# Optimization experiments

Measured on AMD Instinct MI355X. Metric: run time of the kernel, lower is better.

The kernel has to match this reference:

```python
import jax, jax.numpy as jnp
import numpy as np

VOCAB, EMB, HID, NTAG, T = 32000, 1024, 1024, 5, 4096
H2 = HID // 2
START, STOP = 3, 4
NEG = -10000.0


def setup_inputs() -> dict:
    key = jax.random.key(0)
    ks = jax.random.split(key, 14)
    sentence = jax.random.randint(ks[0], (T,), 0, VOCAB)
    emb = jax.random.normal(ks[1], (VOCAB, EMB), jnp.float32) * 0.02
    W_ih_f = jax.random.normal(ks[2], (4 * H2, EMB), jnp.float32) * 0.02
    W_hh_f = jax.random.normal(ks[3], (4 * H2, H2), jnp.float32) * 0.02
    b_f = jax.random.normal(ks[4], (4 * H2,), jnp.float32) * 0.02
    W_ih_b = jax.random.normal(ks[5], (4 * H2, EMB), jnp.float32) * 0.02
    W_hh_b = jax.random.normal(ks[6], (4 * H2, H2), jnp.float32) * 0.02
    b_b = jax.random.normal(ks[7], (4 * H2,), jnp.float32) * 0.02
    W_out = jax.random.normal(ks[8], (NTAG, HID), jnp.float32) * 0.02
    b_out = jax.random.normal(ks[9], (NTAG,), jnp.float32) * 0.02
    transitions = jax.random.normal(ks[10], (NTAG, NTAG), jnp.float32)
    transitions = transitions.at[START, :].set(NEG).at[:, STOP].set(NEG)
    h0 = jax.random.normal(ks[11], (2, 1, H2), jnp.float32)
    c0 = jax.random.normal(ks[12], (2, 1, H2), jnp.float32)
    return dict(sentence=sentence, emb=emb, W_ih_f=W_ih_f, W_hh_f=W_hh_f, b_f=b_f,
                W_ih_b=W_ih_b, W_hh_b=W_hh_b, b_b=b_b, W_out=W_out, b_out=b_out,
                transitions=transitions, h0=h0, c0=c0)


def _lstm_scan(x, h0, c0, W_ih, W_hh, b):
    # x: [T, EMB]; PyTorch gate order i, f, g, o
    def step(carry, xt):
        h, c = carry
        g = W_ih @ xt + W_hh @ h + b  # [4*H2]
        i, f, gg, o = jnp.split(g, 4)
        c2 = jax.nn.sigmoid(f) * c + jax.nn.sigmoid(i) * jnp.tanh(gg)
        h2 = jax.nn.sigmoid(o) * jnp.tanh(c2)
        return (h2, c2), h2
    _, hs = jax.lax.scan(step, (h0, c0), x)
    return hs  # [T, H2]


def _viterbi(feats, transitions):
    init = jnp.full((NTAG,), NEG, jnp.float32).at[START].set(0.0)

    def vstep(fv, feat):
        ntv = fv[None, :] + transitions          # [to, from]
        bptr = jnp.argmax(ntv, axis=1)
        return jnp.max(ntv, axis=1) + feat, bptr

    fv, bptrs = jax.lax.scan(vstep, init, feats)  # bptrs: [T, NTAG]
    terminal = fv + transitions[STOP]
    best_tag = jnp.argmax(terminal)
    score = terminal[best_tag]

    def back(tag, bp):
        prev = bp[tag]
        return prev, prev

    _, path_rev = jax.lax.scan(back, best_tag, bptrs[::-1])
    # path_rev[::-1] = [START, tag_1, ..., tag_{T-1}]; drop START, append best_tag
    path = jnp.concatenate([path_rev[::-1][1:], best_tag[None]])
    return score, path


def reference(sentence, emb, W_ih_f, W_hh_f, b_f, W_ih_b, W_hh_b, b_b,
              W_out, b_out, transitions, h0, c0):
    x = emb[sentence]  # [T, EMB]
    hf = _lstm_scan(x, h0[0, 0], c0[0, 0], W_ih_f, W_hh_f, b_f)
    hb = _lstm_scan(x[::-1], h0[1, 0], c0[1, 0], W_ih_b, W_hh_b, b_b)[::-1]
    lstm_out = jnp.concatenate([hf, hb], axis=-1)          # [T, HID]
    feats = lstm_out @ W_out.T + b_out                     # [T, NTAG]
    score, path = _viterbi(feats, transitions)
    return score, path
```

## Files before the change

### kernel.cpp

```cpp
#include <hip/hip_runtime.h>
#include <hip/hip_bf16.h>
#include <math.h>

#define TSEQ 4096
#define EMBD 1024
#define HH   512
#define NTAGS 5
#define NGATE 2048
#define NEGV (-10000.0f)
#define START_TAG 3
#define STOP_TAG 4
#define LSTM_WGS 64
#define PROJ_WGS 1024
#define VIT_BLOCK (LSTM_WGS + PROJ_WGS)

typedef unsigned long long u64;
typedef unsigned int u32;

__device__ __forceinline__ float sigm(float x){ return 1.0f/(1.0f+expf(-x)); }

__device__ __forceinline__ u64 pack_pair(float h, u32 tag){
  return ((u64)tag << 32) | (u64)__float_as_uint(h);
}
__device__ __forceinline__ float rdlane_f(float v, int l){
  return __uint_as_float((u32)__builtin_amdgcn_readlane(__float_as_uint(v), l));
}

__global__ void k_init(const float* __restrict__ h0, u64* __restrict__ hx2,
                       int* __restrict__ rdy){
  int tid = threadIdx.x;
  if (tid < 1024){
    int dir = tid >> 9, u = tid & 511;
    hx2[(dir*2 + 0)*HH + u] = pack_pair(h0[dir*HH + u], 0u);
    hx2[(dir*2 + 1)*HH + u] = pack_pair(0.f, 0xFFFFFFFFu);
  }
  if (tid < 96) rdy[tid] = 0;
}

__global__ __launch_bounds__(512, 2) void k_fused(
    const int* __restrict__ sent, const float* __restrict__ emb,
    const float* __restrict__ Wif, const float* __restrict__ bf,
    const float* __restrict__ Wib, const float* __restrict__ bb,
    const float* __restrict__ Whf, const float* __restrict__ Whb,
    const float* __restrict__ c0, const float* __restrict__ Wout,
    const float* __restrict__ bout, const float* __restrict__ trans,
    float* __restrict__ A, float* __restrict__ hseq, float* __restrict__ feats,
    int* __restrict__ bpw, float* __restrict__ out,
    u64* __restrict__ hx2, int* __restrict__ rdy){
  __shared__ __align__(16) char smem[17408];
  const int tid = threadIdx.x;

  if (blockIdx.x == VIT_BLOCK){
    if (tid >= 64) return;
    const int lane = tid;
    while (__hip_atomic_load(&rdy[66], __ATOMIC_ACQUIRE, __HIP_MEMORY_SCOPE_AGENT) < LSTM_WGS)
      __builtin_amdgcn_s_sleep(8);
    float*  sf  = (float*)smem;
    float4* sf4 = (float4*)smem;
    const float4* gf4 = (const float4*)feats;
    const int rr = (lane < 5) ? lane : 0;
    const float Tr0 = trans[rr*NTAGS+0], Tr1 = trans[rr*NTAGS+1],
                Tr2 = trans[rr*NTAGS+2], Tr3 = trans[rr*NTAGS+3],
                Tr4 = trans[rr*NTAGS+4];
    const float S0=trans[STOP_TAG*NTAGS+0], S1=trans[STOP_TAG*NTAGS+1],
                S2=trans[STOP_TAG*NTAGS+2], S3=trans[STOP_TAG*NTAGS+3],
                S4=trans[STOP_TAG*NTAGS+4];
    float fv0 = NEGV, fv1 = NEGV, fv2 = NEGV, fv3 = 0.f, fv4 = NEGV;

    for (int c = 0; c < TSEQ/512; c++){
      #pragma unroll
      for (int i = 0; i < 16; i++)
        sf4[i*64 + lane] = gf4[(size_t)c*1024 + i*64 + lane];
      asm volatile("s_waitcnt vmcnt(0) lgkmcnt(0)" ::: "memory");
      for (int tt = 0; tt < 512; tt++){
        const float featr = sf[tt*8 + rr];
        const float n0 = fv0 + Tr0, n1 = fv1 + Tr1, n2 = fv2 + Tr2,
                    n3 = fv3 + Tr3, n4 = fv4 + Tr4;
        const float m  = fmaxf(fmaxf(fmaxf(n0, n1), fmaxf(n2, n3)), n4);
        const int idx  = (n0 == m) ? 0 : ((n1 == m) ? 1 : ((n2 == m) ? 2 :
                         ((n3 == m) ? 3 : 4)));
        const float nf = m + featr;
        fv0 = rdlane_f(nf, 0); fv1 = rdlane_f(nf, 1); fv2 = rdlane_f(nf, 2);
        fv3 = rdlane_f(nf, 3); fv4 = rdlane_f(nf, 4);
        const int i0 = __builtin_amdgcn_readlane(idx, 0);
        const int i1 = __builtin_amdgcn_readlane(idx, 1);
        const int i2 = __builtin_amdgcn_readlane(idx, 2);
        const int i3 = __builtin_amdgcn_readlane(idx, 3);
        const int i4 = __builtin_amdgcn_readlane(idx, 4);
        const int pack = i0 | (i1<<4) | (i2<<8) | (i3<<12) | (i4<<16);
        if (lane == 0) bpw[c*512 + tt] = pack;
      }
    }
    {
      const float n0 = fv0 + S0, n1 = fv1 + S1, n2 = fv2 + S2,
                  n3 = fv3 + S3, n4 = fv4 + S4;
      const float m  = fmaxf(fmaxf(fmaxf(n0, n1), fmaxf(n2, n3)), n4);
      const int btag = (n0 == m) ? 0 : ((n1 == m) ? 1 : ((n2 == m) ? 2 : ((n3 == m) ? 3 : 4)));
      if (lane == 0){ out[0] = m; out[TSEQ] = (float)btag; }
      int tag = btag;
      for (int tb = TSEQ - 1; tb >= 1; tb -= 16){
        int w[16];
        #pragma unroll
        for (int i = 0; i < 16; i++){
          const int t = tb - i;
          w[i] = (t >= 1) ? bpw[t] : 0;
        }
        #pragma unroll
        for (int i = 0; i < 16; i++){
          const int t = tb - i;
          if (t >= 1){
            const int prev = (w[i] >> (tag*4)) & 15;
            if (lane == 0) out[t] = (float)prev;
            tag = prev;
          }
        }
      }
    }
    return;
  }

  if (blockIdx.x >= LSTM_WGS){
    float (*As)[132] = (float(*)[132])smem;
    float (*Bs)[132] = (float(*)[132])(smem + 8448);
    int* srow        = (int*)(smem + 16896);
    const int p   = blockIdx.x - LSTM_WGS;
    const int ti  = p >> 5;
    const int yy  = p & 31;
    const int dir = yy >> 4;
    const int t_tile = dir ? (31 - ti) : ti;
    const int t0  = t_tile * 128;
    const int n0  = (yy & 15) * 128;
    const float* __restrict__ W    = dir ? Wib : Wif;
    const float* __restrict__ bias = dir ? bb : bf;
    if (tid < 128) srow[tid] = sent[t0 + tid];
    __syncthreads();
    const int lr = tid >> 2;
    const int kq = (tid & 3) * 4;
    const float* ea = emb + (size_t)srow[lr]   * EMBD + kq;
    const float* wb = W + (size_t)(n0 + lr)    * EMBD + kq;
    const int tx = tid & 15, ty = tid >> 4;
    float acc[4][8];
    #pragma unroll
    for (int i = 0; i < 4; i++)
      #pragma unroll
      for (int j = 0; j < 8; j++) acc[i][j] = 0.f;

    for (int k0 = 0; k0 < EMBD; k0 += 16){
      float4 va = *(const float4*)(ea + k0);
      float4 vb = *(const float4*)(wb + k0);
      As[kq+0][lr] = va.x; As[kq+1][lr] = va.y; As[kq+2][lr] = va.z; As[kq+3][lr] = va.w;
      Bs[kq+0][lr] = vb.x; Bs[kq+1][lr] = vb.y; Bs[kq+2][lr] = vb.z; Bs[kq+3][lr] = vb.w;
      __syncthreads();
      #pragma unroll
      for (int k = 0; k < 16; k++){
        float a[4], b[8];
        *(float4*)&a[0] = *(const float4*)&As[k][ty*4];
        #pragma unroll
        for (int j = 0; j < 8; j++) b[j] = Bs[k][tx + 16*j];
        #pragma unroll
        for (int i = 0; i < 4; i++)
          #pragma unroll
          for (int j = 0; j < 8; j++)
            acc[i][j] = fmaf(a[i], b[j], acc[i][j]);
      }
      __syncthreads();
    }
    float bj[8];
    #pragma unroll
    for (int j = 0; j < 8; j++) bj[j] = bias[n0 + tx + 16*j];
    float* Abase = A + (size_t)dir * TSEQ * NGATE;
    #pragma unroll
    for (int i = 0; i < 4; i++){
      float* dst = Abase + (size_t)(t0 + ty*4 + i) * NGATE + n0 + tx;
      #pragma unroll
      for (int j = 0; j < 8; j++) dst[16*j] = acc[i][j] + bj[j];
    }
    __syncthreads();
    if (tid == 0)
      __hip_atomic_fetch_add(&rdy[dir*32 + t_tile], 1,
                             __ATOMIC_RELEASE, __HIP_MEMORY_SCOPE_AGENT);
    return;
  }

  float* hlbuf = (float*)smem;
  const int bid  = blockIdx.x;
  const int dir  = bid >> 5;
  const int wg   = bid & 31;
  const int lane = tid & 63;
  const int wv   = tid >> 6;
  const int ul   = tid >> 5;
  const int g    = (tid >> 3) & 3;
  const int q    = tid & 7;
  const int unit = wg*16 + ul;
  const float* __restrict__ Wh = dir ? Whb : Whf;

  float wreg[64];
  {
    const float* wr = Wh + (size_t)(g*HH + unit)*HH + q*64;
    #pragma unroll
    for (int j4 = 0; j4 < 16; j4++){
      float4 vv;
      asm volatile("global_load_dwordx4 %0, %1, off\n\t"
                   "s_waitcnt vmcnt(0)"
                   : "=v"(vv) : "v"(wr + 4*j4) : "memory");
      wreg[4*j4+0]=vv.x; wreg[4*j4+1]=vv.y; wreg[4*j4+2]=vv.z; wreg[4*j4+3]=vv.w;
    }
  }
  float creg = 0.f;
  if (g == 0 && q == 0) creg = c0[dir*HH + unit];

  u64* mb = hx2 + (size_t)dir*2*HH;
  const float* __restrict__ Ab = A + (size_t)dir*TSEQ*NGATE;
  const int sidx = (wv << 6) + lane;

  int cur_tile = (dir ? (TSEQ - 1) : 0) >> 7;
  {
    const int* rf = rdy + dir*32 + cur_tile;
    while (__hip_atomic_load(rf, __ATOMIC_ACQUIRE, __HIP_MEMORY_SCOPE_AGENT) < 16)
      __builtin_amdgcn_s_sleep(2);
  }
  float av = 0.f;
  if (q == 0) av = Ab[(size_t)(dir ? (TSEQ - 1) : 0)*NGATE + g*HH + unit];

  for (int s = 0; s < TSEQ; s++){
    const int t = dir ? (TSEQ - 1 - s) : s;

    {
      u64* src = mb + (size_t)(s & 1)*HH;
      const u32 su = (u32)s;
      u64 v = __hip_atomic_load(&src[sidx], __ATOMIC_RELAXED, __HIP_MEMORY_SCOPE_AGENT);
      while (!__all((u32)(v >> 32) == su)){
        if ((u32)(v >> 32) != su)
          v = __hip_atomic_load(&src[sidx], __ATOMIC_RELAXED, __HIP_MEMORY_SCOPE_AGENT);
      }
      hlbuf[(s & 1)*(8*68) + wv*68 + lane] = __uint_as_float((u32)v);
    }
    __syncthreads();

    float av_next = 0.f;
    if (s + 1 < TSEQ){
      const int t1 = dir ? (TSEQ - 2 - s) : (s + 1);
      const int tile1 = t1 >> 7;
      if (tile1 != cur_tile){
        cur_tile = tile1;
        const int* rf = rdy + dir*32 + tile1;
        while (__hip_atomic_load(rf, __ATOMIC_ACQUIRE, __HIP_MEMORY_SCOPE_AGENT) < 16)
          __builtin_amdgcn_s_sleep(2);
      }
      if (q == 0) av_next = Ab[(size_t)t1*NGATE + g*HH + unit];
    }

    const float* hq = hlbuf + (s & 1)*(8*68) + q*68;
    float p0 = 0.f, p1 = 0.f, p2 = 0.f, p3 = 0.f;
    #pragma unroll
    for (int j4 = 0; j4 < 16; j4++){
      float4 h4 = *(const float4*)(hq + 4*j4);
      p0 = fmaf(wreg[4*j4+0], h4.x, p0);
      p1 = fmaf(wreg[4*j4+1], h4.y, p1);
      p2 = fmaf(wreg[4*j4+2], h4.z, p2);
      p3 = fmaf(wreg[4*j4+3], h4.w, p3);
    }
    float acc = ((p0 + p1) + (p2 + p3)) + av;
    acc += __shfl_xor(acc, 1);
    acc += __shfl_xor(acc, 2);
    acc += __shfl_xor(acc, 4);
    const float act = (g == 2) ? tanhf(acc) : sigm(acc);
    const float f_ = __shfl_down(act, 8);
    const float g_ = __shfl_down(act, 16);
    const float o_ = __shfl_down(act, 24);
    if (g == 0 && q == 0){
      const float c2 = f_*creg + act*g_;
      const float h2 = o_*tanhf(c2);
      creg = c2;
      __hip_atomic_store(&mb[(size_t)((s + 1) & 1)*HH + unit], pack_pair(h2, (u32)(s + 1)),
                         __ATOMIC_RELAXED, __HIP_MEMORY_SCOPE_AGENT);
      hseq[((size_t)dir*TSEQ + t)*HH + unit] = h2;
    }
    av = av_next;
  }

  __syncthreads();
  if (tid == 0)
    __hip_atomic_fetch_add(&rdy[65], 1, __ATOMIC_RELEASE, __HIP_MEMORY_SCOPE_AGENT);
  while (__hip_atomic_load(&rdy[65], __ATOMIC_ACQUIRE, __HIP_MEMORY_SCOPE_AGENT) < LSTM_WGS)
    __builtin_amdgcn_s_sleep(2);
  {
    const int wvi = tid >> 6;
    #pragma unroll
    for (int k = 0; k < 8; k++){
      const int t = bid*64 + wvi*8 + k;
      const float* hf = hseq + (size_t)t*HH;
      const float* hb = hseq + (size_t)(TSEQ + t)*HH;
      float x[16];
      #pragma unroll
      for (int j = 0; j < 8; j++) x[j]     = hf[lane + 64*j];
      #pragma unroll
      for (int j = 0; j < 8; j++) x[8 + j] = hb[lane + 64*j];
      #pragma unroll
      for (int n = 0; n < NTAGS; n++){
        const float* wr = Wout + (size_t)n*(2*HH);
        float p = 0.f;
        #pragma unroll
        for (int j = 0; j < 8; j++) p = fmaf(x[j],     wr[lane + 64*j],      p);
        #pragma unroll
        for (int j = 0; j < 8; j++) p = fmaf(x[8 + j], wr[HH + lane + 64*j], p);
        #pragma unroll
        for (int d = 1; d < 64; d <<= 1) p += __shfl_xor(p, d);
        if (lane == 0) feats[t*8 + n] = p + bout[n];
      }
    }
  }
  __syncthreads();
  if (tid == 0)
    __hip_atomic_fetch_add(&rdy[66], 1, __ATOMIC_RELEASE, __HIP_MEMORY_SCOPE_AGENT);
}

extern "C" void kernel_launch(void* const* d_in, const int* in_sizes, int n_in,
                              void* d_out, int out_size, void* d_ws, size_t ws_size,
                              hipStream_t stream) {
  const int*   sent = (const int*)  d_in[0];
  const float* emb  = (const float*)d_in[1];
  const float* Wihf = (const float*)d_in[2];
  const float* Whhf = (const float*)d_in[3];
  const float* bf_  = (const float*)d_in[4];
  const float* Wihb = (const float*)d_in[5];
  const float* Whhb = (const float*)d_in[6];
  const float* bb_  = (const float*)d_in[7];
  const float* Wout = (const float*)d_in[8];
  const float* bout = (const float*)d_in[9];
  const float* trans= (const float*)d_in[10];
  const float* h0   = (const float*)d_in[11];
  const float* c0   = (const float*)d_in[12];
  float* out = (float*)d_out;

  float* ws   = (float*)d_ws;
  float* A    = ws;
  float* hseq = A    + (size_t)2*TSEQ*NGATE;
  u64*   hx2  = (u64*)(hseq + (size_t)2*TSEQ*HH);
  float* fe   = (float*)(hx2 + 2048);
  int*   bpw  = (int*)(fe + (size_t)TSEQ*8);
  int*   rdy  = bpw + TSEQ;
  (void)ws_size;

  k_init<<<1, 1024, 0, stream>>>(h0, hx2, rdy);
  k_fused<<<VIT_BLOCK + 1, 512, 0, stream>>>(
      sent, emb, Wihf, bf_, Wihb, bb_, Whhf, Whhb, c0, Wout, bout, trans,
      A, hseq, fe, bpw, out, hx2, rdy);
}
```

Measured before the change: 7.672 ms.

## Move Viterbi argmax off serial path and prefetch gate input before h wait

The Viterbi forward loop no longer computes and packs backpointers on each serial step. It stores the forward-variable history to a workspace buffer, then recomputes all backpointers in a parallel pass where each of the 64 lanes handles one timestep. The LSTM recurrence also issues the next step's input-gate load and tile-ready wait before spinning on the hidden-state exchange, so that load latency overlaps the wait. In exchange the forward loop adds a global store per step, and the workspace must hold the extra history buffer.

```diff
diff --git a/kernel.cpp b/kernel.cpp
--- a/kernel.cpp
+++ b/kernel.cpp
@@ -45,7 +45,7 @@
     const float* __restrict__ c0, const float* __restrict__ Wout,
     const float* __restrict__ bout, const float* __restrict__ trans,
     float* __restrict__ A, float* __restrict__ hseq, float* __restrict__ feats,
-    int* __restrict__ bpw, float* __restrict__ out,
+    int* __restrict__ bpw, float* __restrict__ fvh, float* __restrict__ out,
     u64* __restrict__ hx2, int* __restrict__ rdy){
   __shared__ __align__(16) char smem[17408];
   const int tid = threadIdx.x;
@@ -66,6 +66,7 @@
                 S2=trans[STOP_TAG*NTAGS+2], S3=trans[STOP_TAG*NTAGS+3],
                 S4=trans[STOP_TAG*NTAGS+4];
     float fv0 = NEGV, fv1 = NEGV, fv2 = NEGV, fv3 = 0.f, fv4 = NEGV;
+    if (lane < 5) fvh[lane] = (lane == START_TAG) ? 0.f : NEGV;
 
     for (int c = 0; c < TSEQ/512; c++){
       #pragma unroll
@@ -77,26 +78,52 @@
         const float n0 = fv0 + Tr0, n1 = fv1 + Tr1, n2 = fv2 + Tr2,
                     n3 = fv3 + Tr3, n4 = fv4 + Tr4;
         const float m  = fmaxf(fmaxf(fmaxf(n0, n1), fmaxf(n2, n3)), n4);
-        const int idx  = (n0 == m) ? 0 : ((n1 == m) ? 1 : ((n2 == m) ? 2 :
-                         ((n3 == m) ? 3 : 4)));
         const float nf = m + featr;
+        if (lane < 5) fvh[(c*512 + tt + 1)*5 + lane] = nf;
         fv0 = rdlane_f(nf, 0); fv1 = rdlane_f(nf, 1); fv2 = rdlane_f(nf, 2);
         fv3 = rdlane_f(nf, 3); fv4 = rdlane_f(nf, 4);
-        const int i0 = __builtin_amdgcn_readlane(idx, 0);
-        const int i1 = __builtin_amdgcn_readlane(idx, 1);
-        const int i2 = __builtin_amdgcn_readlane(idx, 2);
-        const int i3 = __builtin_amdgcn_readlane(idx, 3);
-        const int i4 = __builtin_amdgcn_readlane(idx, 4);
-        const int pack = i0 | (i1<<4) | (i2<<8) | (i3<<12) | (i4<<16);
-        if (lane == 0) bpw[c*512 + tt] = pack;
-      }
-    }
+      }
+    }
+    int btag;
     {
       const float n0 = fv0 + S0, n1 = fv1 + S1, n2 = fv2 + S2,
                   n3 = fv3 + S3, n4 = fv4 + S4;
       const float m  = fmaxf(fmaxf(fmaxf(n0, n1), fmaxf(n2, n3)), n4);
-      const int btag = (n0 == m) ? 0 : ((n1 == m) ? 1 : ((n2 == m) ? 2 : ((n3 == m) ? 3 : 4)));
+      btag = (n0 == m) ? 0 : ((n1 == m) ? 1 : ((n2 == m) ? 2 : ((n3 == m) ? 3 : 4)));
       if (lane == 0){ out[0] = m; out[TSEQ] = (float)btag; }
+    }
+    asm volatile("s_waitcnt vmcnt(0)" ::: "memory");
+    {
+      const float U00=trans[0],  U01=trans[1],  U02=trans[2],  U03=trans[3],  U04=trans[4];
+      const float U10=trans[5],  U11=trans[6],  U12=trans[7],  U13=trans[8],  U14=trans[9];
+      const float U20=trans[10], U21=trans[11], U22=trans[12], U23=trans[13], U24=trans[14];
+      const float U30=trans[15], U31=trans[16], U32=trans[17], U33=trans[18], U34=trans[19];
+      const float U40=trans[20], U41=trans[21], U42=trans[22], U43=trans[23], U44=trans[24];
+      for (int base = 0; base < TSEQ; base += 64){
+        const int t = base + lane;
+        const float f0 = fvh[t*5+0], f1 = fvh[t*5+1], f2 = fvh[t*5+2],
+                    f3 = fvh[t*5+3], f4 = fvh[t*5+4];
+        int pack;
+#define BROW(Ta,Tb,Tc,Td,Te, OUTI)                                          \
+        {                                                                   \
+          const float n0 = f0 + Ta, n1 = f1 + Tb, n2 = f2 + Tc,             \
+                      n3 = f3 + Td, n4 = f4 + Te;                           \
+          const float m = fmaxf(fmaxf(fmaxf(n0, n1), fmaxf(n2, n3)), n4);   \
+          OUTI = (n0 == m) ? 0 : ((n1 == m) ? 1 : ((n2 == m) ? 2 :          \
+                 ((n3 == m) ? 3 : 4)));                                     \
+        }
+        int i0,i1,i2,i3,i4;
+        BROW(U00,U01,U02,U03,U04, i0)
+        BROW(U10,U11,U12,U13,U14, i1)
+        BROW(U20,U21,U22,U23,U24, i2)
+        BROW(U30,U31,U32,U33,U34, i3)
+        BROW(U40,U41,U42,U43,U44, i4)
+        pack = i0 | (i1<<4) | (i2<<8) | (i3<<12) | (i4<<16);
+        bpw[t] = pack;
+      }
+    }
+    asm volatile("s_waitcnt vmcnt(0)" ::: "memory");
+    {
       int tag = btag;
       for (int tb = TSEQ - 1; tb >= 1; tb -= 16){
         int w[16];
@@ -225,18 +252,6 @@
   for (int s = 0; s < TSEQ; s++){
     const int t = dir ? (TSEQ - 1 - s) : s;
 
-    {
-      u64* src = mb + (size_t)(s & 1)*HH;
-      const u32 su = (u32)s;
-      u64 v = __hip_atomic_load(&src[sidx], __ATOMIC_RELAXED, __HIP_MEMORY_SCOPE_AGENT);
-      while (!__all((u32)(v >> 32) == su)){
-        if ((u32)(v >> 32) != su)
-          v = __hip_atomic_load(&src[sidx], __ATOMIC_RELAXED, __HIP_MEMORY_SCOPE_AGENT);
-      }
-      hlbuf[(s & 1)*(8*68) + wv*68 + lane] = __uint_as_float((u32)v);
-    }
-    __syncthreads();
-
     float av_next = 0.f;
     if (s + 1 < TSEQ){
       const int t1 = dir ? (TSEQ - 2 - s) : (s + 1);
@@ -249,6 +264,18 @@
       }
       if (q == 0) av_next = Ab[(size_t)t1*NGATE + g*HH + unit];
     }
+
+    {
+      u64* src = mb + (size_t)(s & 1)*HH;
+      const u32 su = (u32)s;
+      u64 v = __hip_atomic_load(&src[sidx], __ATOMIC_RELAXED, __HIP_MEMORY_SCOPE_AGENT);
+      while (!__all((u32)(v >> 32) == su)){
+        if ((u32)(v >> 32) != su)
+          v = __hip_atomic_load(&src[sidx], __ATOMIC_RELAXED, __HIP_MEMORY_SCOPE_AGENT);
+      }
+      hlbuf[(s & 1)*(8*68) + wv*68 + lane] = __uint_as_float((u32)v);
+    }
+    __syncthreads();
 
     const float* hq = hlbuf + (s & 1)*(8*68) + q*68;
     float p0 = 0.f, p1 = 0.f, p2 = 0.f, p3 = 0.f;
@@ -340,10 +367,11 @@
   float* fe   = (float*)(hx2 + 2048);
   int*   bpw  = (int*)(fe + (size_t)TSEQ*8);
   int*   rdy  = bpw + TSEQ;
+  float* fvh  = (float*)(rdy + 96);
   (void)ws_size;
 
   k_init<<<1, 1024, 0, stream>>>(h0, hx2, rdy);
   k_fused<<<VIT_BLOCK + 1, 512, 0, stream>>>(
       sent, emb, Wihf, bf_, Wihb, bb_, Whhf, Whhb, c0, Wout, bout, trans,
-      A, hseq, fe, bpw, out, hx2, rdy);
-}
+      A, hseq, fe, bpw, fvh, out, hx2, rdy);
+}
```

After: 9.193 ms. 19.8% more time.
